# Optimization experiments

Measured on AMD Instinct MI355X. Metric: run time of the kernel, lower is better.

The kernel has to match this reference:

```python
import jax, jax.numpy as jnp
import numpy as np

BATCH, IN_DIM, HID_DIM, OUT_DIM, K = 8192, 256, 16384, 256, 256


def setup_inputs() -> dict:
    key = jax.random.key(0)
    k1, k2, k3 = jax.random.split(key, 3)
    x = jax.random.normal(k1, (BATCH, IN_DIM), dtype=jnp.float32)
    # kaiming_uniform-like init scale for encoder/decoder weights
    enc_w = jax.random.normal(k2, (HID_DIM, IN_DIM), dtype=jnp.float32) * (1.0 / np.sqrt(IN_DIM))
    enc_b = jnp.zeros((HID_DIM,), dtype=jnp.float32)
    dec_w = jax.random.normal(k3, (OUT_DIM, HID_DIM), dtype=jnp.float32) * (1.0 / np.sqrt(HID_DIM))
    dec_b = jnp.zeros((OUT_DIM,), dtype=jnp.float32)
    return {"x": x, "enc_w": enc_w, "enc_b": enc_b, "dec_w": dec_w, "dec_b": dec_b, "k": K}


def reference(x, enc_w, enc_b, dec_w, dec_b, k):
    # encoder: [B, in] @ [in, hid] -> [B, hid]
    hidden_pre = x @ enc_w.T + enc_b
    h_relu = jax.nn.relu(hidden_pre)
    kk = min(h_relu.shape[1], int(k))
    # k-th largest value per row as threshold; mask = (x_relu >= threshold)
    topk_vals, _ = jax.lax.top_k(h_relu, kk)          # [B, k]
    thresholds = topk_vals[:, -1:]                    # [B, 1]
    hidden_post = jnp.where(h_relu >= thresholds, h_relu, 0.0)
    # decoder: [B, hid] @ [hid, out] -> [B, out]
    output = hidden_post @ dec_w.T + dec_b
    return (output, hidden_post)
```

## Files before the change

kernel.cpp:

```cpp
#include <hip/hip_runtime.h>
#include <stdint.h>

#define BATCH   8192
#define IN_DIM  256
#define HID_DIM 16384
#define OUT_DIM 256

#define SELCAPF 2048

typedef __attribute__((ext_vector_type(4))) float f32x4;
typedef __attribute__((ext_vector_type(2))) float f32x2;

__device__ __forceinline__ void load_lds_16B(const void* g, void* l) {
  __builtin_amdgcn_global_load_lds(
      (const __attribute__((address_space(1))) unsigned int*)g,
      (__attribute__((address_space(3))) unsigned int*)l, 16, 0, 0);
}
__device__ __forceinline__ float bf16u_to_f(unsigned short u) {
  return __uint_as_float(((unsigned)u) << 16);
}
__device__ __forceinline__ unsigned short f_to_bf16_rne(float f) {
  unsigned u = __float_as_uint(f);
  u += 0x7fffu + ((u >> 16) & 1u);
  return (unsigned short)(u >> 16);
}
__device__ __forceinline__ int read_k(const int* kptr) {
  int k = kptr[0];
  if (k <= 0 || k > 100000000) {
    float kf = __int_as_float(k);
    if (kf >= 1.f && kf <= 16384.f) k = (int)kf;
  }
  if (k < 1) k = 1;
  if (k > HID_DIM) k = HID_DIM;
  return k;
}
__device__ __forceinline__ f32x2 fma2(f32x2 a, f32x2 b, f32x2 c) {
#if __has_builtin(__builtin_elementwise_fma)
  return __builtin_elementwise_fma(a, b, c);
#else
  f32x2 r; r[0] = fmaf(a[0], b[0], c[0]); r[1] = fmaf(a[1], b[1], c[1]); return r;
#endif
}

__global__ __launch_bounds__(256) void k_transb(const float* __restrict__ dec_w,
                                                unsigned short* __restrict__ decT) {
  __shared__ float tile[32][33];
  int j0 = blockIdx.x * 32, o0 = blockIdx.y * 32;
  int tx = threadIdx.x & 31, ty = threadIdx.x >> 5;
#pragma unroll
  for (int rr = 0; rr < 4; rr++)
    tile[ty + rr * 8][tx] = dec_w[(size_t)(o0 + ty + rr * 8) * HID_DIM + (j0 + tx)];
  __syncthreads();
#pragma unroll
  for (int rr = 0; rr < 4; rr++)
    decT[(size_t)(j0 + ty + rr * 8) * OUT_DIM + (o0 + tx)] = f_to_bf16_rne(tile[tx][ty + rr * 8]);
}

__global__ __launch_bounds__(256) void k_transblk(const float* __restrict__ src,
                                                  float* __restrict__ dst) {
  __shared__ float tile[32][33];
  const int r0 = blockIdx.x * 32, k0 = blockIdx.y * 32;
  const int tx = threadIdx.x & 31, ty = threadIdx.x >> 5;
#pragma unroll
  for (int rr = 0; rr < 4; rr++)
    tile[ty + rr * 8][tx] = src[(size_t)(r0 + ty + rr * 8) * IN_DIM + (k0 + tx)];
  __syncthreads();
  const int blk = r0 >> 7, rin = r0 & 127;
#pragma unroll
  for (int rr = 0; rr < 4; rr++) {
    const int kk = k0 + ty + rr * 8;
    dst[((size_t)blk * IN_DIM + kk) * 128 + rin + tx] = tile[tx][ty + rr * 8];
  }
}

__global__ __launch_bounds__(256, 4) void k_gemm_pk2(const float* __restrict__ XT,
                                                     const float* __restrict__ WT,
                                                     const float* __restrict__ encb,
                                                     float* __restrict__ hid) {
  __shared__ __align__(16) float As[32 * 128];
  __shared__ __align__(16) float Bs[32 * 128];
  const int bn = blockIdx.x, bm = blockIdx.y;
  const int t = threadIdx.x, w = t >> 6, lane = t & 63;
  const int tx = t & 15, ty = t >> 4;

  f32x2 acc[8][4] = {};

  const float* Abase = XT + (size_t)bm * (IN_DIM * 128);
  const float* Bbase = WT + (size_t)bn * (IN_DIM * 128);

  for (int k0 = 0; k0 < IN_DIM; k0 += 32) {
#pragma unroll
    for (int o = 0; o < 4; o++) {
      const int i = w * 4 + o;
      load_lds_16B(Abase + k0 * 128 + i * 256 + lane * 4, &As[i * 256]);
      load_lds_16B(Bbase + k0 * 128 + i * 256 + lane * 4, &Bs[i * 256]);
    }
    __syncthreads();
#pragma unroll 8
    for (int kk = 0; kk < 32; kk++) {
      const f32x4 av0 = *(const f32x4*)&As[kk * 128 + ty * 8];
      const f32x4 av1 = *(const f32x4*)&As[kk * 128 + ty * 8 + 4];
      const f32x4 bv0 = *(const f32x4*)&Bs[kk * 128 + tx * 8];
      const f32x4 bv1 = *(const f32x4*)&Bs[kk * 128 + tx * 8 + 4];
      f32x2 b2[4];
      b2[0] = __builtin_shufflevector(bv0, bv0, 0, 1);
      b2[1] = __builtin_shufflevector(bv0, bv0, 2, 3);
      b2[2] = __builtin_shufflevector(bv1, bv1, 0, 1);
      b2[3] = __builtin_shufflevector(bv1, bv1, 2, 3);
#pragma unroll
      for (int i = 0; i < 8; i++) {
        const float asc = (i < 4) ? av0[i & 3] : av1[i & 3];
        f32x2 ai; ai[0] = asc; ai[1] = asc;
#pragma unroll
        for (int j = 0; j < 4; j++)
          acc[i][j] = fma2(ai, b2[j], acc[i][j]);
      }
    }
    __syncthreads();
  }

#pragma unroll
  for (int i = 0; i < 8; i++) {
    const int m = bm * 128 + ty * 8 + i;
    float o[8];
#pragma unroll
    for (int j = 0; j < 4; j++) {
      const float h0 = acc[i][j][0] + encb[bn * 128 + tx * 8 + j * 2];
      const float h1 = acc[i][j][1] + encb[bn * 128 + tx * 8 + j * 2 + 1];
      o[j * 2]     = (h0 > 0.f) ? h0 : 0.f;
      o[j * 2 + 1] = (h1 > 0.f) ? h1 : 0.f;
    }
    float* dst = &hid[(size_t)m * HID_DIM + bn * 128 + tx * 8];
    *(float4*)dst = *(float4*)&o[0];
    *(float4*)(dst + 4) = *(float4*)&o[4];
  }
}

__global__ __launch_bounds__(256) void k_topk3(const unsigned short* __restrict__ decTb,
                                               const float* __restrict__ decb,
                                               const int* __restrict__ kptr,
                                               float* __restrict__ out,
                                               float* __restrict__ hid) {
  __shared__ unsigned hist[8][257];
  __shared__ unsigned cums[257];
  __shared__ float selV[SELCAPF];
  __shared__ unsigned short selI[SELCAPF];
  __shared__ unsigned s_selcnt, s_b, s_need;
  __shared__ int s_keepall;

  const int r = blockIdx.x, t = threadIdx.x;
  float* hrow = hid + (size_t)r * HID_DIM;
  const int k = read_k(kptr);

  f32x4 row[16];
#pragma unroll
  for (int c = 0; c < 16; c++) row[c] = *(const f32x4*)&hrow[(c * 256 + t) * 4];

  for (int i = t; i < 8 * 257; i += 256) ((unsigned*)hist)[i] = 0u;
  if (t == 0) { s_selcnt = 0; s_keepall = 0; }
  __syncthreads();

#pragma unroll
  for (int c = 0; c < 16; c++)
#pragma unroll
    for (int e = 0; e < 4; e++) {
      const unsigned b = __float_as_uint(row[c][e]) >> 24;
      if (b) atomicAdd(&hist[t & 7][b], 1u);
    }
  __syncthreads();
  { unsigned s = 0;
#pragma unroll
    for (int cpy = 0; cpy < 8; cpy++) s += hist[cpy][t];
    cums[t] = s; }
  __syncthreads();
  for (int off = 1; off < 256; off <<= 1) {
    const unsigned v = cums[t];
    const unsigned a = (t + off < 256) ? cums[t + off] : 0u;
    __syncthreads();
    cums[t] = v + a;
    __syncthreads();
  }
  if (t == 0 && cums[1] < (unsigned)k) s_keepall = 1;
  if (t >= 1) {
    const unsigned incl = cums[t], excl = (t < 255) ? cums[t + 1] : 0u;
    if (incl >= (unsigned)k && excl < (unsigned)k) { s_b = (unsigned)t; s_need = (unsigned)k - excl; }
  }
  __syncthreads();

  unsigned prefix = 0;
  const int keepall = s_keepall;
  if (!keepall) {
    prefix = s_b << 24;
    unsigned need = s_need;
    for (int pass = 0; pass < 3; pass++) {
      const int shift = 16 - pass * 8;
      for (int i = t; i < 8 * 257; i += 256) ((unsigned*)hist)[i] = 0u;
      __syncthreads();
      const unsigned pfx = prefix;
      const int pshift = shift + 8;
#pragma unroll
      for (int c = 0; c < 16; c++)
#pragma unroll
        for (int e = 0; e < 4; e++) {
          const unsigned bits = __float_as_uint(row[c][e]);
          if ((bits >> pshift) == (pfx >> pshift))
            atomicAdd(&hist[t & 7][(bits >> shift) & 255u], 1u);
        }
      __syncthreads();
      { unsigned s = 0;
#pragma unroll
        for (int cpy = 0; cpy < 8; cpy++) s += hist[cpy][t];
        cums[t] = s; }
      __syncthreads();
      for (int off = 1; off < 256; off <<= 1) {
        const unsigned v = cums[t];
        const unsigned a = (t + off < 256) ? cums[t + off] : 0u;
        __syncthreads();
        cums[t] = v + a;
        __syncthreads();
      }
      { const unsigned incl = cums[t], excl = (t < 255) ? cums[t + 1] : 0u;
        if (incl >= need && excl < need) { s_b = (unsigned)t; s_need = need - excl; } }
      __syncthreads();
      prefix |= s_b << shift;
      need = s_need;
      __syncthreads();
    }
  }
  const unsigned T = prefix;

#pragma unroll
  for (int c = 0; c < 16; c++) {
    const int base = (c * 256 + t) * 4;
    f32x4 o;
#pragma unroll
    for (int e = 0; e < 4; e++) {
      const float v = row[c][e];
      const unsigned bits = __float_as_uint(v);
      const bool keep = keepall || (bits >= T);
      o[e] = keep ? v : 0.f;
      if (keep && bits != 0u) {
        const unsigned p = atomicAdd(&s_selcnt, 1u);
        if (p < SELCAPF) { selV[p] = v; selI[p] = (unsigned short)(base + e); }
      }
    }
    *(f32x4*)&hrow[base] = o;
  }
  __syncthreads();

  const unsigned nsel = s_selcnt;
  float a0 = decb[t], a1 = 0.f, a2 = 0.f, a3 = 0.f;
  if (nsel <= SELCAPF) {
    unsigned s = 0;
    for (; s + 4 <= nsel; s += 4) {
      a0 += selV[s + 0] * bf16u_to_f(decTb[(size_t)selI[s + 0] * OUT_DIM + t]);
      a1 += selV[s + 1] * bf16u_to_f(decTb[(size_t)selI[s + 1] * OUT_DIM + t]);
      a2 += selV[s + 2] * bf16u_to_f(decTb[(size_t)selI[s + 2] * OUT_DIM + t]);
      a3 += selV[s + 3] * bf16u_to_f(decTb[(size_t)selI[s + 3] * OUT_DIM + t]);
    }
    for (; s < nsel; s++)
      a0 += selV[s] * bf16u_to_f(decTb[(size_t)selI[s] * OUT_DIM + t]);
  } else {
    for (int j = 0; j < HID_DIM; j++) {
      const float hv = hrow[j];
      if (hv != 0.f) a0 += hv * bf16u_to_f(decTb[(size_t)j * OUT_DIM + t]);
    }
  }
  out[(size_t)r * OUT_DIM + t] = (a0 + a1) + (a2 + a3);
}

__global__ __launch_bounds__(256, 4) void k_gemm_pk(const float* __restrict__ X,
                                                    const float* __restrict__ W,
                                                    const float* __restrict__ encb,
                                                    float* __restrict__ hid) {
  __shared__ float As[32][132];
  __shared__ float Bs[32][132];
  const int bn = blockIdx.x, bm = blockIdx.y;
  const int t = threadIdx.x;
  const int tx = t & 15, ty = t >> 4;
  const int sr = t & 127, sh = t >> 7;
  f32x2 acc[8][4] = {};
  const float* Ab = X + (size_t)(bm * 128) * IN_DIM;
  const float* Bb = W + (size_t)(bn * 128) * IN_DIM;
  for (int k0 = 0; k0 < IN_DIM; k0 += 32) {
#pragma unroll
    for (int q = 0; q < 4; q++) {
      const int ko = sh * 16 + q * 4;
      const float4 av = *(const float4*)&Ab[(size_t)sr * IN_DIM + k0 + ko];
      As[ko + 0][sr] = av.x; As[ko + 1][sr] = av.y;
      As[ko + 2][sr] = av.z; As[ko + 3][sr] = av.w;
      const float4 bv = *(const float4*)&Bb[(size_t)sr * IN_DIM + k0 + ko];
      Bs[ko + 0][sr] = bv.x; Bs[ko + 1][sr] = bv.y;
      Bs[ko + 2][sr] = bv.z; Bs[ko + 3][sr] = bv.w;
    }
    __syncthreads();
#pragma unroll 8
    for (int kk = 0; kk < 32; kk++) {
      const f32x4 av0 = *(const f32x4*)&As[kk][ty * 8];
      const f32x4 av1 = *(const f32x4*)&As[kk][ty * 8 + 4];
      const f32x4 bv0 = *(const f32x4*)&Bs[kk][tx * 8];
      const f32x4 bv1 = *(const f32x4*)&Bs[kk][tx * 8 + 4];
      f32x2 b2[4];
      b2[0] = __builtin_shufflevector(bv0, bv0, 0, 1);
      b2[1] = __builtin_shufflevector(bv0, bv0, 2, 3);
      b2[2] = __builtin_shufflevector(bv1, bv1, 0, 1);
      b2[3] = __builtin_shufflevector(bv1, bv1, 2, 3);
#pragma unroll
      for (int i = 0; i < 8; i++) {
        const float asc = (i < 4) ? av0[i & 3] : av1[i & 3];
        f32x2 ai; ai[0] = asc; ai[1] = asc;
#pragma unroll
        for (int j = 0; j < 4; j++) acc[i][j] = fma2(ai, b2[j], acc[i][j]);
      }
    }
    __syncthreads();
  }
#pragma unroll
  for (int i = 0; i < 8; i++) {
    const int m = bm * 128 + ty * 8 + i;
    float o[8];
#pragma unroll
    for (int j = 0; j < 4; j++) {
      const float h0 = acc[i][j][0] + encb[bn * 128 + tx * 8 + j * 2];
      const float h1 = acc[i][j][1] + encb[bn * 128 + tx * 8 + j * 2 + 1];
      o[j * 2] = (h0 > 0.f) ? h0 : 0.f;
      o[j * 2 + 1] = (h1 > 0.f) ? h1 : 0.f;
    }
    float* dst = &hid[(size_t)m * HID_DIM + bn * 128 + tx * 8];
    *(float4*)dst = *(float4*)&o[0];
    *(float4*)(dst + 4) = *(float4*)&o[4];
  }
}

__global__ __launch_bounds__(256) void k_topkf(const float* __restrict__ dec,
                                               const float* __restrict__ decb,
                                               const int* __restrict__ kptr,
                                               float* __restrict__ out,
                                               float* __restrict__ hid) {
  __shared__ unsigned hist[8][257];
  __shared__ unsigned tot[256];
  __shared__ float selV[SELCAPF];
  __shared__ unsigned short selI[SELCAPF];
  __shared__ unsigned s_selcnt, s_need, s_pref, s_byte;
  __shared__ int s_keepall;
  const int r = blockIdx.x, t = threadIdx.x;
  float* hrow = hid + (size_t)r * HID_DIM;
  const int k = read_k(kptr);
  for (int i = t; i < 8 * 257; i += 256) ((unsigned*)hist)[i] = 0u;
  if (t == 0) { s_selcnt = 0; s_keepall = 0; s_pref = 0; }
  __syncthreads();
#pragma unroll
  for (int c = 0; c < 16; c++) {
    const f32x4 v = *(const f32x4*)&hrow[(c * 256 + t) * 4];
#pragma unroll
    for (int e = 0; e < 4; e++) {
      const unsigned b = __float_as_uint(v[e]) >> 24;
      if (b) atomicAdd(&hist[t & 7][b], 1u);
    }
  }
  __syncthreads();
  { unsigned s = 0;
#pragma unroll
    for (int c = 0; c < 8; c++) s += hist[c][t];
    tot[t] = s; }
  __syncthreads();
  if (t == 0) {
    unsigned cum = 0; int b1 = -1; unsigned need = 0;
    for (int b = 255; b >= 1; b--) {
      const unsigned c = tot[b];
      if (cum + c >= (unsigned)k) { b1 = b; need = (unsigned)k - cum; break; }
      cum += c;
    }
    if (b1 < 0) s_keepall = 1;
    else { s_pref = ((unsigned)b1) << 24; s_need = need; }
  }
  __syncthreads();
  if (!s_keepall) {
    for (int pass = 1; pass <= 3; pass++) {
      const int shift = 24 - pass * 8;
      tot[t] = 0;
      __syncthreads();
      const unsigned prefhi = s_pref >> (shift + 8);
#pragma unroll
      for (int c = 0; c < 16; c++) {
        const f32x4 v = *(const f32x4*)&hrow[(c * 256 + t) * 4];
#pragma unroll
        for (int e = 0; e < 4; e++) {
          const unsigned bits = __float_as_uint(v[e]);
          if ((bits >> (shift + 8)) == prefhi) atomicAdd(&tot[(bits >> shift) & 255u], 1u);
        }
      }
      __syncthreads();
      if (t == 0) {
        unsigned cum = 0; const unsigned need = s_need;
        for (int b = 255; b >= 0; b--) {
          const unsigned c = tot[b];
          if (cum + c >= need) { s_byte = (unsigned)b; s_need = need - cum; break; }
          cum += c;
        }
        s_pref |= s_byte << shift;
      }
      __syncthreads();
    }
  }
  const int keepall = s_keepall;
  const unsigned T = s_pref;
#pragma unroll
  for (int c = 0; c < 16; c++) {
    const int base = (c * 256 + t) * 4;
    const f32x4 v = *(const f32x4*)&hrow[base];
    f32x4 o;
#pragma unroll
    for (int e = 0; e < 4; e++) {
      const unsigned bits = __float_as_uint(v[e]);
      const bool keep = keepall || (bits >= T);
      o[e] = keep ? v[e] : 0.f;
      if (keep && bits != 0u) {
        const unsigned p = atomicAdd(&s_selcnt, 1u);
        if (p < SELCAPF) { selV[p] = v[e]; selI[p] = (unsigned short)(base + e); }
      }
    }
    *(f32x4*)&hrow[base] = o;
  }
  __syncthreads();
  const unsigned nsel = s_selcnt;
  float a0 = decb[t], a1 = 0.f, a2 = 0.f, a3 = 0.f;
  if (nsel <= SELCAPF) {
    unsigned s = 0;
    for (; s + 4 <= nsel; s += 4) {
#pragma unroll
      for (int u = 0; u < 4; u++) {
        const unsigned idx = selI[s + u];
        (u == 0 ? a0 : u == 1 ? a1 : u == 2 ? a2 : a3) += selV[s + u] * dec[(size_t)t * HID_DIM + idx];
      }
    }
    for (; s < nsel; s++)
      a0 += selV[s] * dec[(size_t)t * HID_DIM + selI[s]];
  } else {
    for (int j = 0; j < HID_DIM; j++) {
      const float hv = hrow[j];
      if (hv != 0.f) a0 += hv * dec[(size_t)t * HID_DIM + j];
    }
  }
  out[(size_t)r * OUT_DIM + t] = (a0 + a1) + (a2 + a3);
}

extern "C" void kernel_launch(void* const* d_in, const int* in_sizes, int n_in,
                              void* d_out, int out_size, void* d_ws, size_t ws_size,
                              hipStream_t stream) {
  int ix = 0, iew = 1, ieb = 2, idw = 3, idb = 4, ik = 5;
  if (n_in >= 6 && in_sizes[0] == OUT_DIM && in_sizes[5] == BATCH * IN_DIM) {
    idb = 0; idw = 1; ieb = 2; iew = 3; ik = 4; ix = 5;
  }
  const float* x     = (const float*)d_in[ix];
  const float* enc_w = (const float*)d_in[iew];
  const float* enc_b = (const float*)d_in[ieb];
  const float* dec_w = (const float*)d_in[idw];
  const float* dec_b = (const float*)d_in[idb];
  const int*   kptr  = (const int*)d_in[ik];

  float* out = (float*)d_out;
  float* hid = out + (size_t)BATCH * OUT_DIM;

  const size_t B_decT = (size_t)HID_DIM * OUT_DIM * 2;
  const size_t B_XT   = (size_t)BATCH * IN_DIM * 4;
  const size_t B_WT   = (size_t)HID_DIM * IN_DIM * 4;
  const size_t need = 64 + B_decT + B_XT + B_WT;

  if (ws_size >= need) {
    unsigned char* p = (unsigned char*)d_ws;
    unsigned short* decTb = (unsigned short*)(p + 64);
    float* XT = (float*)(p + 64 + B_decT);
    float* WT = (float*)(p + 64 + B_decT + B_XT);
    k_transblk<<<dim3(BATCH / 32, IN_DIM / 32), 256, 0, stream>>>(x, XT);
    k_transblk<<<dim3(HID_DIM / 32, IN_DIM / 32), 256, 0, stream>>>(enc_w, WT);
    k_transb<<<dim3(HID_DIM / 32, OUT_DIM / 32), 256, 0, stream>>>(dec_w, decTb);
    k_gemm_pk2<<<dim3(HID_DIM / 128, BATCH / 128), 256, 0, stream>>>(XT, WT, enc_b, hid);
    k_topk3<<<dim3(BATCH), 256, 0, stream>>>(decTb, dec_b, kptr, out, hid);
  } else {
    k_gemm_pk<<<dim3(HID_DIM / 128, BATCH / 128), 256, 0, stream>>>(x, enc_w, enc_b, hid);
    k_topkf<<<dim3(BATCH), 256, 0, stream>>>(dec_w, dec_b, kptr, out, hid);
  }
}
```

Baseline: 1.498 ms.

## Duplicate X into pairs for packed-FMA GEMM and streamline top-k radix select

Adds a transpose kernel that writes X duplicated element-wise, so the encoder GEMM can feed packed f32x2 FMAs directly from LDS with wide loads and no per-element broadcast. The top-k kernel swaps the LDS Hillis-Steele prefix scan, which needs many barriers, for a wave-shuffle suffix scan. It also compacts the candidates that match the top byte into LDS, so later radix passes scan only those few values instead of the whole register row. The cost is twice the workspace and bandwidth for X, more LDS in the GEMM with occupancy lowered to 3, and a fallback path when candidates overflow.

After: 1.609 ms. 1.07x slower.

```diff
diff --git a/kernel.cpp b/kernel.cpp
--- a/kernel.cpp
+++ b/kernel.cpp
@@ -7,6 +7,7 @@
 #define OUT_DIM 256
 
 #define SELCAPF 2048
+#define CANDCAP 2048
 
 typedef __attribute__((ext_vector_type(4))) float f32x4;
 typedef __attribute__((ext_vector_type(2))) float f32x2;
@@ -42,6 +43,23 @@
 #endif
 }
 
+__device__ __forceinline__ unsigned suffix_incl(unsigned c, int t, unsigned* wtot) {
+  const int lane = t & 63, w = t >> 6;
+  unsigned s = c;
+#pragma unroll
+  for (int off = 1; off < 64; off <<= 1) {
+    unsigned v = __shfl_down(s, off);
+    if (lane + off < 64) s += v;
+  }
+  if (lane == 0) wtot[w] = s;
+  __syncthreads();
+  unsigned r = s;
+#pragma unroll
+  for (int w2 = 1; w2 < 4; w2++)
+    if (w2 > w) r += wtot[w2];
+  return r;
+}
+
 __global__ __launch_bounds__(256) void k_transb(const float* __restrict__ dec_w,
                                                 unsigned short* __restrict__ decT) {
   __shared__ float tile[32][33];
@@ -70,6 +88,99 @@
   for (int rr = 0; rr < 4; rr++) {
     const int kk = k0 + ty + rr * 8;
     dst[((size_t)blk * IN_DIM + kk) * 128 + rin + tx] = tile[tx][ty + rr * 8];
+  }
+}
+
+__global__ __launch_bounds__(256) void k_transdup(const float* __restrict__ src,
+                                                  float* __restrict__ dst) {
+  __shared__ float tile[32][33];
+  const int r0 = blockIdx.x * 32, k0 = blockIdx.y * 32;
+  const int tx = threadIdx.x & 31, ty = threadIdx.x >> 5;
+#pragma unroll
+  for (int rr = 0; rr < 4; rr++)
+    tile[ty + rr * 8][tx] = src[(size_t)(r0 + ty + rr * 8) * IN_DIM + (k0 + tx)];
+  __syncthreads();
+  const int blk = r0 >> 7, rin = r0 & 127;
+#pragma unroll
+  for (int rr = 0; rr < 4; rr++) {
+    const int kk = k0 + ty + rr * 8;
+    const float v = tile[tx][ty + rr * 8];
+    float2 d; d.x = v; d.y = v;
+    *(float2*)&dst[((size_t)blk * IN_DIM + kk) * 256 + 2 * (rin + tx)] = d;
+  }
+}
+
+__global__ __launch_bounds__(256, 3) void k_gemm_pk3(const float* __restrict__ XTd,
+                                                     const float* __restrict__ WT,
+                                                     const float* __restrict__ encb,
+                                                     float* __restrict__ hid) {
+  __shared__ __align__(16) float As[32 * 256];
+  __shared__ __align__(16) float Bs[32 * 128];
+  const int bn = blockIdx.x, bm = blockIdx.y;
+  const int t = threadIdx.x, w = t >> 6, lane = t & 63;
+  const int tx = t & 15, ty = t >> 4;
+
+  f32x2 acc[8][4] = {};
+
+  const float* Abase = XTd + (size_t)bm * (IN_DIM * 256);
+  const float* Bbase = WT + (size_t)bn * (IN_DIM * 128);
+
+  for (int k0 = 0; k0 < IN_DIM; k0 += 32) {
+#pragma unroll
+    for (int o = 0; o < 8; o++) {
+      const int i = w * 8 + o;
+      load_lds_16B(Abase + k0 * 256 + i * 256 + lane * 4, &As[i * 256]);
+    }
+#pragma unroll
+    for (int o = 0; o < 4; o++) {
+      const int i = w * 4 + o;
+      load_lds_16B(Bbase + k0 * 128 + i * 256 + lane * 4, &Bs[i * 256]);
+    }
+    __syncthreads();
+#pragma unroll 8
+    for (int kk = 0; kk < 32; kk++) {
+      const f32x4 ad0 = *(const f32x4*)&As[kk * 256 + ty * 16];
+      const f32x4 ad1 = *(const f32x4*)&As[kk * 256 + ty * 16 + 4];
+      const f32x4 ad2 = *(const f32x4*)&As[kk * 256 + ty * 16 + 8];
+      const f32x4 ad3 = *(const f32x4*)&As[kk * 256 + ty * 16 + 12];
+      const f32x4 bv0 = *(const f32x4*)&Bs[kk * 128 + tx * 8];
+      const f32x4 bv1 = *(const f32x4*)&Bs[kk * 128 + tx * 8 + 4];
+      f32x2 a2[8], b2[4];
+      a2[0] = __builtin_shufflevector(ad0, ad0, 0, 1);
+      a2[1] = __builtin_shufflevector(ad0, ad0, 2, 3);
+      a2[2] = __builtin_shufflevector(ad1, ad1, 0, 1);
+      a2[3] = __builtin_shufflevector(ad1, ad1, 2, 3);
+      a2[4] = __builtin_shufflevector(ad2, ad2, 0, 1);
+      a2[5] = __builtin_shufflevector(ad2, ad2, 2, 3);
+      a2[6] = __builtin_shufflevector(ad3, ad3, 0, 1);
+      a2[7] = __builtin_shufflevector(ad3, ad3, 2, 3);
+      b2[0] = __builtin_shufflevector(bv0, bv0, 0, 1);
+      b2[1] = __builtin_shufflevector(bv0, bv0, 2, 3);
+      b2[2] = __builtin_shufflevector(bv1, bv1, 0, 1);
+      b2[3] = __builtin_shufflevector(bv1, bv1, 2, 3);
+#pragma unroll
+      for (int i = 0; i < 8; i++)
+#pragma unroll
+        for (int j = 0; j < 4; j++)
+          acc[i][j] = fma2(a2[i], b2[j], acc[i][j]);
+    }
+    __syncthreads();
+  }
+
+#pragma unroll
+  for (int i = 0; i < 8; i++) {
+    const int m = bm * 128 + ty * 8 + i;
+    float o[8];
+#pragma unroll
+    for (int j = 0; j < 4; j++) {
+      const float h0 = acc[i][j][0] + encb[bn * 128 + tx * 8 + j * 2];
+      const float h1 = acc[i][j][1] + encb[bn * 128 + tx * 8 + j * 2 + 1];
+      o[j * 2]     = (h0 > 0.f) ? h0 : 0.f;
+      o[j * 2 + 1] = (h1 > 0.f) ? h1 : 0.f;
+    }
+    float* dst = &hid[(size_t)m * HID_DIM + bn * 128 + tx * 8];
+    *(float4*)dst = *(float4*)&o[0];
+    *(float4*)(dst + 4) = *(float4*)&o[4];
   }
 }
 
@@ -136,16 +247,17 @@
   }
 }
 
-__global__ __launch_bounds__(256) void k_topk3(const unsigned short* __restrict__ decTb,
+__global__ __launch_bounds__(256) void k_topk6(const unsigned short* __restrict__ decTb,
                                                const float* __restrict__ decb,
                                                const int* __restrict__ kptr,
                                                float* __restrict__ out,
                                                float* __restrict__ hid) {
   __shared__ unsigned hist[8][257];
-  __shared__ unsigned cums[257];
+  __shared__ unsigned wtot[4];
+  __shared__ unsigned candB[CANDCAP];
   __shared__ float selV[SELCAPF];
   __shared__ unsigned short selI[SELCAPF];
-  __shared__ unsigned s_selcnt, s_b, s_need;
+  __shared__ unsigned s_selcnt, s_cnt, s_b, s_need;
   __shared__ int s_keepall;
 
   const int r = blockIdx.x, t = threadIdx.x;
@@ -157,7 +269,7 @@
   for (int c = 0; c < 16; c++) row[c] = *(const f32x4*)&hrow[(c * 256 + t) * 4];
 
   for (int i = t; i < 8 * 257; i += 256) ((unsigned*)hist)[i] = 0u;
-  if (t == 0) { s_selcnt = 0; s_keepall = 0; }
+  if (t == 0) { s_selcnt = 0; s_cnt = 0; s_keepall = 0; }
   __syncthreads();
 
 #pragma unroll
@@ -168,66 +280,78 @@
       if (b) atomicAdd(&hist[t & 7][b], 1u);
     }
   __syncthreads();
+  unsigned cme;
   { unsigned s = 0;
 #pragma unroll
     for (int cpy = 0; cpy < 8; cpy++) s += hist[cpy][t];
-    cums[t] = s; }
-  __syncthreads();
-  for (int off = 1; off < 256; off <<= 1) {
-    const unsigned v = cums[t];
-    const unsigned a = (t + off < 256) ? cums[t + off] : 0u;
+    cme = s; }
+  {
+    const unsigned S = suffix_incl(cme, t, wtot);
+    if (t == 1 && S < (unsigned)k) s_keepall = 1;
+    if (t >= 1 && cme > 0 && S >= (unsigned)k && S - cme < (unsigned)k) {
+      s_b = (unsigned)t; s_need = (unsigned)k - (S - cme);
+    }
+  }
+  __syncthreads();
+
+  const int keepall = s_keepall;
+  unsigned T = 0u;
+  if (!keepall) {
+    unsigned prefix = s_b;
+    unsigned need = s_need;
+#pragma unroll
+    for (int c = 0; c < 16; c++)
+#pragma unroll
+      for (int e = 0; e < 4; e++) {
+        const unsigned bits = __float_as_uint(row[c][e]);
+        if ((bits >> 24) == prefix) {
+          const unsigned p = atomicAdd(&s_cnt, 1u);
+          if (p < CANDCAP) candB[p] = bits;
+        }
+      }
     __syncthreads();
-    cums[t] = v + a;
-    __syncthreads();
-  }
-  if (t == 0 && cums[1] < (unsigned)k) s_keepall = 1;
-  if (t >= 1) {
-    const unsigned incl = cums[t], excl = (t < 255) ? cums[t + 1] : 0u;
-    if (incl >= (unsigned)k && excl < (unsigned)k) { s_b = (unsigned)t; s_need = (unsigned)k - excl; }
-  }
-  __syncthreads();
-
-  unsigned prefix = 0;
-  const int keepall = s_keepall;
-  if (!keepall) {
-    prefix = s_b << 24;
-    unsigned need = s_need;
+    const unsigned n = s_cnt;
+    const int useCand = (n <= CANDCAP);
+
     for (int pass = 0; pass < 3; pass++) {
       const int shift = 16 - pass * 8;
+      const int pshift = shift + 8;
       for (int i = t; i < 8 * 257; i += 256) ((unsigned*)hist)[i] = 0u;
       __syncthreads();
-      const unsigned pfx = prefix;
-      const int pshift = shift + 8;
-#pragma unroll
-      for (int c = 0; c < 16; c++)
-#pragma unroll
-        for (int e = 0; e < 4; e++) {
-          const unsigned bits = __float_as_uint(row[c][e]);
-          if ((bits >> pshift) == (pfx >> pshift))
+      if (useCand) {
+        for (unsigned i = t; i < n; i += 256) {
+          const unsigned bits = candB[i];
+          if ((bits >> pshift) == prefix)
             atomicAdd(&hist[t & 7][(bits >> shift) & 255u], 1u);
         }
+      } else {
+#pragma unroll
+        for (int c = 0; c < 16; c++)
+#pragma unroll
+          for (int e = 0; e < 4; e++) {
+            const unsigned bits = __float_as_uint(row[c][e]);
+            if ((bits >> pshift) == prefix)
+              atomicAdd(&hist[t & 7][(bits >> shift) & 255u], 1u);
+          }
+      }
       __syncthreads();
       { unsigned s = 0;
 #pragma unroll
         for (int cpy = 0; cpy < 8; cpy++) s += hist[cpy][t];
-        cums[t] = s; }
+        cme = s; }
+      {
+        const unsigned S = suffix_incl(cme, t, wtot);
+        if (cme > 0 && S >= need && S - cme < need) {
+          s_b = (unsigned)t; s_need = need - (S - cme);
+        }
+      }
       __syncthreads();
-      for (int off = 1; off < 256; off <<= 1) {
-        const unsigned v = cums[t];
-        const unsigned a = (t + off < 256) ? cums[t + off] : 0u;
-        __syncthreads();
-        cums[t] = v + a;
-        __syncthreads();
-      }
-      { const unsigned incl = cums[t], excl = (t < 255) ? cums[t + 1] : 0u;
-        if (incl >= need && excl < need) { s_b = (unsigned)t; s_need = need - excl; } }
-      __syncthreads();
-      prefix |= s_b << shift;
+      prefix = (prefix << 8) | s_b;
       need = s_need;
       __syncthreads();
     }
-  }
-  const unsigned T = prefix;
+    T = prefix;
+  }
 
 #pragma unroll
   for (int c = 0; c < 16; c++) {
@@ -464,10 +588,22 @@
 
   const size_t B_decT = (size_t)HID_DIM * OUT_DIM * 2;
   const size_t B_XT   = (size_t)BATCH * IN_DIM * 4;
+  const size_t B_XTd  = (size_t)BATCH * IN_DIM * 8;
   const size_t B_WT   = (size_t)HID_DIM * IN_DIM * 4;
-  const size_t need = 64 + B_decT + B_XT + B_WT;
-
-  if (ws_size >= need) {
+  const size_t needA = 64 + B_decT + B_XTd + B_WT;
+  const size_t needB = 64 + B_decT + B_XT + B_WT;
+
+  if (ws_size >= needA) {
+    unsigned char* p = (unsigned char*)d_ws;
+    unsigned short* decTb = (unsigned short*)(p + 64);
+    float* XTd = (float*)(p + 64 + B_decT);
+    float* WT  = (float*)(p + 64 + B_decT + B_XTd);
+    k_transdup<<<dim3(BATCH / 32, IN_DIM / 32), 256, 0, stream>>>(x, XTd);
+    k_transblk<<<dim3(HID_DIM / 32, IN_DIM / 32), 256, 0, stream>>>(enc_w, WT);
+    k_transb<<<dim3(HID_DIM / 32, OUT_DIM / 32), 256, 0, stream>>>(dec_w, decTb);
+    k_gemm_pk3<<<dim3(HID_DIM / 128, BATCH / 128), 256, 0, stream>>>(XTd, WT, enc_b, hid);
+    k_topk6<<<dim3(BATCH), 256, 0, stream>>>(decTb, dec_b, kptr, out, hid);
+  } else if (ws_size >= needB) {
     unsigned char* p = (unsigned char*)d_ws;
     unsigned short* decTb = (unsigned short*)(p + 64);
     float* XT = (float*)(p + 64 + B_decT);
@@ -476,7 +612,7 @@
     k_transblk<<<dim3(HID_DIM / 32, IN_DIM / 32), 256, 0, stream>>>(enc_w, WT);
     k_transb<<<dim3(HID_DIM / 32, OUT_DIM / 32), 256, 0, stream>>>(dec_w, decTb);
     k_gemm_pk2<<<dim3(HID_DIM / 128, BATCH / 128), 256, 0, stream>>>(XT, WT, enc_b, hid);
-    k_topk3<<<dim3(BATCH), 256, 0, stream>>>(decTb, dec_b, kptr, out, hid);
+    k_topk6<<<dim3(BATCH), 256, 0, stream>>>(decTb, dec_b, kptr, out, hid);
   } else {
     k_gemm_pk<<<dim3(HID_DIM / 128, BATCH / 128), 256, 0, stream>>>(x, enc_w, enc_b, hid);
     k_topkf<<<dim3(BATCH), 256, 0, stream>>>(dec_w, dec_b, kptr, out, hid);
```

## Use split-bf16 MFMA encoder GEMM with fp32 recheck of near-threshold top-k candidates

Applied to the files above, without the earlier changes.

Replaces the fp32 FMA encoder GEMM with a three-term bf16 hi/lo split computed on MFMA instructions, preceded by a split kernel that stores hi and lo bf16 planes of x and enc_w instead of transposing them. To guard top-k selection against the small error of the split product, the top-k kernel recomputes in exact fp32 the hidden values that fall inside a narrow window around the threshold and re-ranks them to decide which to keep. This moves the dominant GEMM onto matrix cores. In exchange it adds extra per-row dot products and a linear search over the candidate list in the mask pass, and it falls back to the plain threshold when the window holds too many candidates.

New measurement: 1.320 ms. -11.9%, faster.

```diff
diff --git a/kernel.cpp b/kernel.cpp
--- a/kernel.cpp
+++ b/kernel.cpp
@@ -7,9 +7,12 @@
 #define OUT_DIM 256
 
 #define SELCAPF 2048
-
-typedef __attribute__((ext_vector_type(4))) float f32x4;
-typedef __attribute__((ext_vector_type(2))) float f32x2;
+#define BCAP    128
+
+typedef __attribute__((ext_vector_type(8))) __bf16 bf16x8;
+typedef __attribute__((ext_vector_type(4))) float  f32x4;
+typedef __attribute__((ext_vector_type(2))) float  f32x2;
+typedef __attribute__((ext_vector_type(8))) unsigned short u16x8;
 
 __device__ __forceinline__ void load_lds_16B(const void* g, void* l) {
   __builtin_amdgcn_global_load_lds(
@@ -42,6 +45,27 @@
 #endif
 }
 
+__global__ __launch_bounds__(256) void k_split(const float* __restrict__ src,
+                                               unsigned short* __restrict__ hi,
+                                               unsigned short* __restrict__ lo,
+                                               int n8) {
+  const int i = blockIdx.x * 256 + threadIdx.x;
+  if (i >= n8) return;
+  const int base = i * 8;
+  const f32x4 a = *(const f32x4*)&src[base];
+  const f32x4 b = *(const f32x4*)&src[base + 4];
+  u16x8 h, l;
+#pragma unroll
+  for (int e = 0; e < 4; e++) {
+    { const float v = a[e]; const unsigned short hb = f_to_bf16_rne(v);
+      h[e] = hb; l[e] = f_to_bf16_rne(v - bf16u_to_f(hb)); }
+    { const float v = b[e]; const unsigned short hb = f_to_bf16_rne(v);
+      h[e + 4] = hb; l[e + 4] = f_to_bf16_rne(v - bf16u_to_f(hb)); }
+  }
+  *(u16x8*)&hi[base] = h;
+  *(u16x8*)&lo[base] = l;
+}
+
 __global__ __launch_bounds__(256) void k_transb(const float* __restrict__ dec_w,
                                                 unsigned short* __restrict__ decT) {
   __shared__ float tile[32][33];
@@ -56,96 +80,103 @@
     decT[(size_t)(j0 + ty + rr * 8) * OUT_DIM + (o0 + tx)] = f_to_bf16_rne(tile[tx][ty + rr * 8]);
 }
 
-__global__ __launch_bounds__(256) void k_transblk(const float* __restrict__ src,
-                                                  float* __restrict__ dst) {
-  __shared__ float tile[32][33];
-  const int r0 = blockIdx.x * 32, k0 = blockIdx.y * 32;
-  const int tx = threadIdx.x & 31, ty = threadIdx.x >> 5;
-#pragma unroll
-  for (int rr = 0; rr < 4; rr++)
-    tile[ty + rr * 8][tx] = src[(size_t)(r0 + ty + rr * 8) * IN_DIM + (k0 + tx)];
-  __syncthreads();
-  const int blk = r0 >> 7, rin = r0 & 127;
-#pragma unroll
-  for (int rr = 0; rr < 4; rr++) {
-    const int kk = k0 + ty + rr * 8;
-    dst[((size_t)blk * IN_DIM + kk) * 128 + rin + tx] = tile[tx][ty + rr * 8];
-  }
-}
-
-__global__ __launch_bounds__(256, 4) void k_gemm_pk2(const float* __restrict__ XT,
-                                                     const float* __restrict__ WT,
-                                                     const float* __restrict__ encb,
-                                                     float* __restrict__ hid) {
-  __shared__ __align__(16) float As[32 * 128];
-  __shared__ __align__(16) float Bs[32 * 128];
+__global__ __launch_bounds__(256) void k_gemm3(const unsigned short* __restrict__ Xh,
+                                               const unsigned short* __restrict__ Xl,
+                                               const unsigned short* __restrict__ Wh,
+                                               const unsigned short* __restrict__ Wl,
+                                               const float* __restrict__ encb,
+                                               float* __restrict__ hid) {
+  __shared__ __align__(16) unsigned short Ash[128 * 64];
+  __shared__ __align__(16) unsigned short Asl[128 * 64];
+  __shared__ __align__(16) unsigned short Bsh[128 * 64];
+  __shared__ __align__(16) unsigned short Bsl[128 * 64];
+
   const int bn = blockIdx.x, bm = blockIdx.y;
   const int t = threadIdx.x, w = t >> 6, lane = t & 63;
-  const int tx = t & 15, ty = t >> 4;
-
-  f32x2 acc[8][4] = {};
-
-  const float* Abase = XT + (size_t)bm * (IN_DIM * 128);
-  const float* Bbase = WT + (size_t)bn * (IN_DIM * 128);
-
-  for (int k0 = 0; k0 < IN_DIM; k0 += 32) {
+  const int wm = w >> 1, wn = w & 1;
+  f32x4 acc[4][4] = {};
+
+  const int lrow8 = lane >> 3;
+  const int cblk  = (lane & 7) ^ lrow8;
+
+  const size_t aoff = (size_t)(bm * 128) * IN_DIM;
+  const size_t boff = (size_t)(bn * 128) * IN_DIM;
+
+  for (int kb = 0; kb < 4; kb++) {
 #pragma unroll
     for (int o = 0; o < 4; o++) {
-      const int i = w * 4 + o;
-      load_lds_16B(Abase + k0 * 128 + i * 256 + lane * 4, &As[i * 256]);
-      load_lds_16B(Bbase + k0 * 128 + i * 256 + lane * 4, &Bs[i * 256]);
-    }
-    __syncthreads();
-#pragma unroll 8
-    for (int kk = 0; kk < 32; kk++) {
-      const f32x4 av0 = *(const f32x4*)&As[kk * 128 + ty * 8];
-      const f32x4 av1 = *(const f32x4*)&As[kk * 128 + ty * 8 + 4];
-      const f32x4 bv0 = *(const f32x4*)&Bs[kk * 128 + tx * 8];
-      const f32x4 bv1 = *(const f32x4*)&Bs[kk * 128 + tx * 8 + 4];
-      f32x2 b2[4];
-      b2[0] = __builtin_shufflevector(bv0, bv0, 0, 1);
-      b2[1] = __builtin_shufflevector(bv0, bv0, 2, 3);
-      b2[2] = __builtin_shufflevector(bv1, bv1, 0, 1);
-      b2[3] = __builtin_shufflevector(bv1, bv1, 2, 3);
-#pragma unroll
-      for (int i = 0; i < 8; i++) {
-        const float asc = (i < 4) ? av0[i & 3] : av1[i & 3];
-        f32x2 ai; ai[0] = asc; ai[1] = asc;
-#pragma unroll
-        for (int j = 0; j < 4; j++)
-          acc[i][j] = fma2(ai, b2[j], acc[i][j]);
-      }
-    }
-    __syncthreads();
-  }
-
-#pragma unroll
-  for (int i = 0; i < 8; i++) {
-    const int m = bm * 128 + ty * 8 + i;
-    float o[8];
-#pragma unroll
-    for (int j = 0; j < 4; j++) {
-      const float h0 = acc[i][j][0] + encb[bn * 128 + tx * 8 + j * 2];
-      const float h1 = acc[i][j][1] + encb[bn * 128 + tx * 8 + j * 2 + 1];
-      o[j * 2]     = (h0 > 0.f) ? h0 : 0.f;
-      o[j * 2 + 1] = (h1 > 0.f) ? h1 : 0.f;
-    }
-    float* dst = &hid[(size_t)m * HID_DIM + bn * 128 + tx * 8];
-    *(float4*)dst = *(float4*)&o[0];
-    *(float4*)(dst + 4) = *(float4*)&o[4];
-  }
-}
-
-__global__ __launch_bounds__(256) void k_topk3(const unsigned short* __restrict__ decTb,
+      const int R = (w * 4 + o) * 8;
+      const size_t go = (size_t)(R + lrow8) * IN_DIM + kb * 64 + cblk * 8;
+      load_lds_16B(Xh + aoff + go, &Ash[(w * 4 + o) * 512]);
+      load_lds_16B(Xl + aoff + go, &Asl[(w * 4 + o) * 512]);
+      load_lds_16B(Wh + boff + go, &Bsh[(w * 4 + o) * 512]);
+      load_lds_16B(Wl + boff + go, &Bsl[(w * 4 + o) * 512]);
+    }
+    __syncthreads();
+#pragma unroll
+    for (int ks = 0; ks < 2; ks++) {
+      bf16x8 ah[4], al[4], bh[4], bl[4];
+#pragma unroll
+      for (int i = 0; i < 4; i++) {
+        const int row = wm * 64 + i * 16 + (lane & 15);
+        const int c   = (ks * 4 + (lane >> 4)) ^ (row & 7);
+        ah[i] = *(const bf16x8*)&Ash[row * 64 + c * 8];
+        al[i] = *(const bf16x8*)&Asl[row * 64 + c * 8];
+      }
+#pragma unroll
+      for (int j = 0; j < 4; j++) {
+        const int row = wn * 64 + j * 16 + (lane & 15);
+        const int c   = (ks * 4 + (lane >> 4)) ^ (row & 7);
+        bh[j] = *(const bf16x8*)&Bsh[row * 64 + c * 8];
+        bl[j] = *(const bf16x8*)&Bsl[row * 64 + c * 8];
+      }
+#pragma unroll
+      for (int i = 0; i < 4; i++)
+#pragma unroll
+        for (int j = 0; j < 4; j++) {
+          acc[i][j] = __builtin_amdgcn_mfma_f32_16x16x32_bf16(al[i], bh[j], acc[i][j], 0, 0, 0);
+          acc[i][j] = __builtin_amdgcn_mfma_f32_16x16x32_bf16(ah[i], bl[j], acc[i][j], 0, 0, 0);
+          acc[i][j] = __builtin_amdgcn_mfma_f32_16x16x32_bf16(ah[i], bh[j], acc[i][j], 0, 0, 0);
+        }
+    }
+    __syncthreads();
+  }
+
+#pragma unroll
+  for (int j = 0; j < 4; j++) {
+    const int gc = bn * 128 + wn * 64 + j * 16 + (lane & 15);
+    const float eb = encb[gc];
+#pragma unroll
+    for (int i = 0; i < 4; i++) {
+      const int gr0 = bm * 128 + wm * 64 + i * 16 + ((lane >> 4) << 2);
+#pragma unroll
+      for (int rg = 0; rg < 4; rg++) {
+        float h = acc[i][j][rg] + eb;
+        h = (h > 0.f) ? h : 0.f;
+        hid[(size_t)(gr0 + rg) * HID_DIM + gc] = h;
+      }
+    }
+  }
+}
+
+__global__ __launch_bounds__(256) void k_topk7(const float* __restrict__ X,
+                                               const float* __restrict__ encw,
+                                               const float* __restrict__ encb,
+                                               const unsigned short* __restrict__ decTb,
                                                const float* __restrict__ decb,
                                                const int* __restrict__ kptr,
                                                float* __restrict__ out,
                                                float* __restrict__ hid) {
   __shared__ unsigned hist[8][257];
   __shared__ unsigned cums[257];
+  __shared__ float xrow[IN_DIM];
+  __shared__ int bidx[BCAP];
+  __shared__ float chv[BCAP];
+  __shared__ unsigned char bkeep[BCAP];
   __shared__ float selV[SELCAPF];
   __shared__ unsigned short selI[SELCAPF];
-  __shared__ unsigned s_selcnt, s_b, s_need;
+  __shared__ unsigned s_selcnt, s_b, s_need, s_bcnt, s_m;
+  __shared__ float s_tau;
   __shared__ int s_keepall;
 
   const int r = blockIdx.x, t = threadIdx.x;
@@ -156,8 +187,9 @@
 #pragma unroll
   for (int c = 0; c < 16; c++) row[c] = *(const f32x4*)&hrow[(c * 256 + t) * 4];
 
+  xrow[t] = X[(size_t)r * IN_DIM + t];
   for (int i = t; i < 8 * 257; i += 256) ((unsigned*)hist)[i] = 0u;
-  if (t == 0) { s_selcnt = 0; s_keepall = 0; }
+  if (t == 0) { s_selcnt = 0; s_keepall = 0; s_bcnt = 0; s_m = 0; s_tau = -1.f; }
   __syncthreads();
 
 #pragma unroll
@@ -229,6 +261,67 @@
   }
   const unsigned T = prefix;
 
+  float wloB = 1.0f, whiB = -1.0f;
+  int mode = keepall ? 0 : 2;
+  if (!keepall) {
+    const float Tf = __uint_as_float(T);
+    const float delta = 1e-3f + Tf * 1e-3f;
+    wloB = Tf - delta; whiB = Tf + delta;
+    unsigned mloc = 0;
+#pragma unroll
+    for (int c = 0; c < 16; c++)
+#pragma unroll
+      for (int e = 0; e < 4; e++) {
+        const float v = row[c][e];
+        if (v > whiB) mloc++;
+        else if (v >= wloB && v > 0.f) {
+          const unsigned p = atomicAdd(&s_bcnt, 1u);
+          if (p < BCAP) bidx[p] = (c * 256 + t) * 4 + e;
+        }
+      }
+    if (mloc) atomicAdd(&s_m, mloc);
+  }
+  __syncthreads();
+  const unsigned bcnt = s_bcnt;
+  if (!keepall && (bcnt == 0 || bcnt > BCAP || wloB <= 0.f)) mode = 1;
+
+  if (mode == 2) {
+    if (t < (int)bcnt) {
+      const int j = bidx[t];
+      const float* wr = encw + (size_t)j * IN_DIM;
+      float acc = 0.f;
+      for (int kk = 0; kk < IN_DIM; kk += 8) {
+        const f32x4 w0 = *(const f32x4*)&wr[kk];
+        const f32x4 w1 = *(const f32x4*)&wr[kk + 4];
+        acc = fmaf(xrow[kk + 0], w0[0], acc);
+        acc = fmaf(xrow[kk + 1], w0[1], acc);
+        acc = fmaf(xrow[kk + 2], w0[2], acc);
+        acc = fmaf(xrow[kk + 3], w0[3], acc);
+        acc = fmaf(xrow[kk + 4], w1[0], acc);
+        acc = fmaf(xrow[kk + 5], w1[1], acc);
+        acc = fmaf(xrow[kk + 6], w1[2], acc);
+        acc = fmaf(xrow[kk + 7], w1[3], acc);
+      }
+      acc += encb[j];
+      acc = (acc > 0.f) ? acc : 0.f;
+      chv[t] = acc;
+    }
+    __syncthreads();
+    const unsigned need = (unsigned)k - s_m;
+    if (t < (int)bcnt) {
+      const float v = chv[t];
+      unsigned g = 0, e = 0;
+      for (unsigned m2 = 0; m2 < bcnt; m2++) {
+        const float u = chv[m2];
+        g += (u > v); e += (u == v);
+      }
+      if (g < need && need <= g + e) s_tau = v;
+    }
+    __syncthreads();
+    if (t < (int)bcnt) bkeep[t] = (chv[t] >= s_tau) ? 1 : 0;
+    __syncthreads();
+  }
+
 #pragma unroll
   for (int c = 0; c < 16; c++) {
     const int base = (c * 256 + t) * 4;
@@ -237,7 +330,18 @@
     for (int e = 0; e < 4; e++) {
       const float v = row[c][e];
       const unsigned bits = __float_as_uint(v);
-      const bool keep = keepall || (bits >= T);
+      bool keep;
+      if (mode == 0) keep = true;
+      else if (mode == 1) keep = (bits >= T);
+      else {
+        if (v > whiB) keep = true;
+        else if (v < wloB || v <= 0.f) keep = false;
+        else {
+          keep = false;
+          for (unsigned m2 = 0; m2 < bcnt; m2++)
+            if (bidx[m2] == base + e) { keep = (bkeep[m2] != 0); break; }
+        }
+      }
       o[e] = keep ? v : 0.f;
       if (keep && bits != 0u) {
         const unsigned p = atomicAdd(&s_selcnt, 1u);
@@ -463,20 +567,23 @@
   float* hid = out + (size_t)BATCH * OUT_DIM;
 
   const size_t B_decT = (size_t)HID_DIM * OUT_DIM * 2;
-  const size_t B_XT   = (size_t)BATCH * IN_DIM * 4;
-  const size_t B_WT   = (size_t)HID_DIM * IN_DIM * 4;
-  const size_t need = 64 + B_decT + B_XT + B_WT;
+  const size_t B_xpl  = (size_t)BATCH * IN_DIM * 2;
+  const size_t B_wpl  = (size_t)HID_DIM * IN_DIM * 2;
+  const size_t need = 64 + B_decT + 2 * B_xpl + 2 * B_wpl;
 
   if (ws_size >= need) {
     unsigned char* p = (unsigned char*)d_ws;
     unsigned short* decTb = (unsigned short*)(p + 64);
-    float* XT = (float*)(p + 64 + B_decT);
-    float* WT = (float*)(p + 64 + B_decT + B_XT);
-    k_transblk<<<dim3(BATCH / 32, IN_DIM / 32), 256, 0, stream>>>(x, XT);
-    k_transblk<<<dim3(HID_DIM / 32, IN_DIM / 32), 256, 0, stream>>>(enc_w, WT);
+    unsigned short* xhi = (unsigned short*)(p + 64 + B_decT);
+    unsigned short* xlo = (unsigned short*)(p + 64 + B_decT + B_xpl);
+    unsigned short* wHi = (unsigned short*)(p + 64 + B_decT + 2 * B_xpl);
+    unsigned short* wLo = (unsigned short*)(p + 64 + B_decT + 2 * B_xpl + B_wpl);
+
+    k_split<<<dim3((BATCH * IN_DIM / 8 + 255) / 256), 256, 0, stream>>>(x, xhi, xlo, BATCH * IN_DIM / 8);
+    k_split<<<dim3((HID_DIM * IN_DIM / 8 + 255) / 256), 256, 0, stream>>>(enc_w, wHi, wLo, HID_DIM * IN_DIM / 8);
     k_transb<<<dim3(HID_DIM / 32, OUT_DIM / 32), 256, 0, stream>>>(dec_w, decTb);
-    k_gemm_pk2<<<dim3(HID_DIM / 128, BATCH / 128), 256, 0, stream>>>(XT, WT, enc_b, hid);
-    k_topk3<<<dim3(BATCH), 256, 0, stream>>>(decTb, dec_b, kptr, out, hid);
+    k_gemm3<<<dim3(HID_DIM / 128, BATCH / 128), 256, 0, stream>>>(xhi, xlo, wHi, wLo, enc_b, hid);
+    k_topk7<<<dim3(BATCH), 256, 0, stream>>>(x, enc_w, enc_b, decTb, dec_b, kptr, out, hid);
   } else {
     k_gemm_pk<<<dim3(HID_DIM / 128, BATCH / 128), 256, 0, stream>>>(x, enc_w, enc_b, hid);
     k_topkf<<<dim3(BATCH), 256, 0, stream>>>(dec_w, dec_b, kptr, out, hid);
```
